# Kernel tuning notes

Measured on AMD Instinct MI355X. Metric: run time of the kernel, lower is better.

## Reference

```python
import jax, jax.numpy as jnp
import numpy as np

N_NODES = 100000
N_EDGES = 1600000
F = 64
UNITS = 64


def setup_inputs() -> dict:
    key = jax.random.key(0)
    k = jax.random.split(key, 8)
    x = jax.random.normal(k[0], (N_NODES, F), dtype=jnp.float32)
    edge_index = jax.random.randint(k[1], (2, N_EDGES), 0, N_NODES, dtype=jnp.int32)
    edge_weight = jnp.ones((N_EDGES,), dtype=jnp.float32)
    # glorot-uniform-ish params
    def glorot(kk, shape):
        lim = np.sqrt(6.0 / (shape[0] + shape[1]))
        return jax.random.uniform(kk, shape, dtype=jnp.float32, minval=-lim, maxval=lim)
    mlp_kernel = glorot(k[2], (F, UNITS))
    mlp_bias = jnp.zeros((UNITS,), dtype=jnp.float32)
    neighs_kernel = glorot(k[3], (UNITS, UNITS))
    self_kernel = glorot(k[4], (F, UNITS))
    bias = jnp.zeros((2 * UNITS,), dtype=jnp.float32)
    return {"x": x, "edge_index": edge_index, "edge_weight": edge_weight,
            "mlp_kernel": mlp_kernel, "mlp_bias": mlp_bias,
            "neighs_kernel": neighs_kernel, "self_kernel": self_kernel, "bias": bias}


def reference(x, edge_index, edge_weight, mlp_kernel, mlp_bias, neighs_kernel, self_kernel, bias):
    num_nodes = x.shape[0]
    row, col = edge_index[0], edge_index[1]
    # gcn_mapper: neighbor message scaled by edge weight (original forces weights to 1)
    neighbor_x = x[col] * edge_weight[:, None]            # [E, F]
    h = jax.nn.relu(neighbor_x @ mlp_kernel + mlp_bias)   # [E, U]
    # unsorted_segment_mean over destination row (empty segments -> 0, matching TF)
    seg_sum = jax.ops.segment_sum(h, row, num_segments=num_nodes)              # [N, U]
    cnt = jax.ops.segment_sum(jnp.ones_like(row, dtype=h.dtype), row, num_segments=num_nodes)
    reduced_h = seg_sum / jnp.maximum(cnt, 1.0)[:, None]
    from_neighs = reduced_h @ neighs_kernel               # [N, U]
    from_x = x @ self_kernel                              # [N, U]
    out = jnp.concatenate([from_neighs, from_x], axis=1) + bias
    out = jax.nn.relu(out)                                # [N, 2U]
    return out
```

## Files before the change

### kernel.cpp

```cpp
#include <hip/hip_runtime.h>

#define MAXSLICE 12544
#define MAXSUB   800
#define NBH 32
#define IDXCAP 512

static __device__ __forceinline__ float relu_f(float v) { return fmaxf(v, 0.f); }

static __device__ __forceinline__ unsigned short f2bf(float f) {
  unsigned u = __float_as_uint(f);
  u += 0x7fffu + ((u >> 16) & 1u);
  return (unsigned short)(u >> 16);
}
static __device__ __forceinline__ float bf2f(unsigned short h) {
  return __uint_as_float(((unsigned)h) << 16);
}

__global__ __launch_bounds__(256) void k_node_dual_gemm(
    const float* __restrict__ x, const float* __restrict__ mk,
    const float* __restrict__ sk, const float* __restrict__ bias,
    unsigned short* __restrict__ xwh, float* __restrict__ out, int n_nodes)
{
  __shared__ float s_mk[64][64];
  __shared__ float s_sk[64][64];
  __shared__ float s_xT[64][68];
  const int tid = threadIdx.x;
  for (int i = tid; i < 4096; i += 256) {
    s_mk[i >> 6][i & 63] = mk[i];
    s_sk[i >> 6][i & 63] = sk[i];
  }
  const int node0 = blockIdx.x * 64;
  for (int i = tid; i < 4096; i += 256) {
    int nl = i >> 6, f = i & 63;
    int n = node0 + nl;
    s_xT[f][nl] = (n < n_nodes) ? x[(size_t)n * 64 + f] : 0.f;
  }
  __syncthreads();
  const int g  = tid >> 4;
  const int ub = (tid & 15) * 4;
  float am[4][4] = {{0.f}};
  float as[4][4] = {{0.f}};
  for (int f = 0; f < 64; ++f) {
    float4 wm = *(const float4*)&s_mk[f][ub];
    float4 ws = *(const float4*)&s_sk[f][ub];
    float4 xv = *(const float4*)&s_xT[f][4 * g];
    const float xs[4] = {xv.x, xv.y, xv.z, xv.w};
#pragma unroll
    for (int j = 0; j < 4; ++j) {
      am[j][0] += xs[j] * wm.x; am[j][1] += xs[j] * wm.y;
      am[j][2] += xs[j] * wm.z; am[j][3] += xs[j] * wm.w;
      as[j][0] += xs[j] * ws.x; as[j][1] += xs[j] * ws.y;
      as[j][2] += xs[j] * ws.z; as[j][3] += xs[j] * ws.w;
    }
  }
  float4 bv = *(const float4*)&bias[64 + ub];
#pragma unroll
  for (int j = 0; j < 4; ++j) {
    int n = node0 + 4 * g + j;
    if (n >= n_nodes) break;
    ushort4 o1 = make_ushort4(f2bf(am[j][0]), f2bf(am[j][1]),
                              f2bf(am[j][2]), f2bf(am[j][3]));
    *(ushort4*)&xwh[(size_t)n * 64 + ub] = o1;
    *(float4*)&out[(size_t)n * 128 + 64 + ub] =
        make_float4(relu_f(as[j][0] + bv.x), relu_f(as[j][1] + bv.y),
                    relu_f(as[j][2] + bv.z), relu_f(as[j][3] + bv.w));
  }
}

__global__ __launch_bounds__(256) void k_count(
    const int* __restrict__ row, int* __restrict__ cnt, int n_edges)
{
  int e = blockIdx.x * 256 + threadIdx.x;
  if (e < n_edges) atomicAdd(&cnt[row[e]], 1);
}

__global__ __launch_bounds__(256) void k_build_sliced(
    const int* __restrict__ row, const int* __restrict__ col,
    const float* __restrict__ ew, int* __restrict__ off,
    int2* __restrict__ elist, int n_edges, int n_nodes)
{
  const int slice = blockIdx.x & 7;
  const int vb    = blockIdx.x >> 3;
  const int nvb   = gridDim.x >> 3;
  const int sliceN = (n_nodes + 7) >> 3;
  const int lo = slice * sliceN;
  const int hi = min(lo + sliceN, n_nodes);
  for (int e = vb * 256 + threadIdx.x; e < n_edges; e += nvb * 256) {
    int r = row[e];
    if (r >= lo && r < hi) {
      int pos = atomicAdd(&off[r], 1);
      elist[pos] = make_int2(col[e], __float_as_int(ew[e]));
    }
  }
}

__global__ __launch_bounds__(1024) void k_bsum(
    const int* __restrict__ cnt, int* __restrict__ bsum, int n)
{
  __shared__ int s[1024];
  int tid = threadIdx.x;
  int i = blockIdx.x * 1024 + tid;
  s[tid] = (i < n) ? cnt[i] : 0;
  __syncthreads();
  for (int d = 512; d > 0; d >>= 1) {
    if (tid < d) s[tid] += s[tid + d];
    __syncthreads();
  }
  if (tid == 0) bsum[blockIdx.x] = s[0];
}

__global__ __launch_bounds__(1024) void k_boffs(
    const int* __restrict__ cnt, const int* __restrict__ bsum,
    int* __restrict__ off, int n, int nb)
{
  __shared__ int s[1024];
  __shared__ int sp[128];
  int tid = threadIdx.x;
  if (tid < 128) {
    int acc = 0;
    for (int j = tid; j < blockIdx.x && j < nb; j += 128) acc += bsum[j];
    sp[tid] = acc;
  }
  int i = blockIdx.x * 1024 + tid;
  int v = (i < n) ? cnt[i] : 0;
  s[tid] = v;
  __syncthreads();
  for (int d = 64; d > 0; d >>= 1) {
    if (tid < d) sp[tid] += sp[tid + d];
    __syncthreads();
  }
  for (int d = 1; d < 1024; d <<= 1) {
    int t = (tid >= d) ? s[tid - d] : 0;
    __syncthreads();
    s[tid] += t;
    __syncthreads();
  }
  if (i < n) off[i] = s[tid] - v + sp[0];
}

__global__ __launch_bounds__(256) void k_bin(
    const int* __restrict__ row, const int* __restrict__ col,
    const float* __restrict__ ew,
    int* __restrict__ brow, int2* __restrict__ bpair,
    int* __restrict__ bcur, int n_edges, int sliceN, int cap)
{
  __shared__ int  s_wcnt[4][8];
  __shared__ int  s_tot[8];
  __shared__ int  s_toff[8];
  __shared__ int  s_gaddr[8];
  __shared__ int  s_rowst[1024];
  __shared__ int2 s_pairst[1024];
  const int tid  = threadIdx.x;
  const int wave = tid >> 6;
  const int lane = tid & 63;
  const unsigned usliceN = (unsigned)sliceN;
  const int stride = gridDim.x * 1024;
  for (int e0 = blockIdx.x * 1024; e0 < n_edges; e0 += stride) {
    const int e = e0 + 4 * tid;
    int   rr[4], cc[4];
    float ww[4];
    int   ss[4];
    if (e + 3 < n_edges) {
      int4 r4   = *(const int4*)&row[e];
      int4 c4   = *(const int4*)&col[e];
      float4 w4 = *(const float4*)&ew[e];
      rr[0] = r4.x; rr[1] = r4.y; rr[2] = r4.z; rr[3] = r4.w;
      cc[0] = c4.x; cc[1] = c4.y; cc[2] = c4.z; cc[3] = c4.w;
      ww[0] = w4.x; ww[1] = w4.y; ww[2] = w4.z; ww[3] = w4.w;
#pragma unroll
      for (int j = 0; j < 4; ++j) ss[j] = (int)((unsigned)rr[j] / usliceN);
    } else {
#pragma unroll
      for (int j = 0; j < 4; ++j) {
        int ej = e + j;
        bool v = ej < n_edges;
        rr[j] = v ? row[ej] : 0;
        cc[j] = v ? col[ej] : 0;
        ww[j] = v ? ew[ej]  : 0.f;
        ss[j] = v ? (int)((unsigned)rr[j] / usliceN) : -1;
      }
    }
#pragma unroll
    for (int b = 0; b < 8; ++b) {
      int c = 0;
#pragma unroll
      for (int j = 0; j < 4; ++j) c += __popcll(__ballot(ss[j] == b));
      if (lane == 0) s_wcnt[wave][b] = c;
    }
    __syncthreads();
    if (wave == 0 && lane < 8) {
      const int b = lane;
      int t0 = s_wcnt[0][b], t1 = s_wcnt[1][b], t2 = s_wcnt[2][b], t3 = s_wcnt[3][b];
      int tot = t0 + t1 + t2 + t3;
      s_tot[b] = tot;
      s_wcnt[0][b] = 0;
      s_wcnt[1][b] = t0;
      s_wcnt[2][b] = t0 + t1;
      s_wcnt[3][b] = t0 + t1 + t2;
      int gbase = tot ? atomicAdd(&bcur[b], tot) : 0;
      int pre = 0;
#pragma unroll
      for (int j2 = 0; j2 < 8; ++j2) pre += (j2 < b) ? s_tot[j2] : 0;
      s_toff[b]  = pre;
      s_gaddr[b] = b * cap + gbase - pre;
    }
    __syncthreads();
#pragma unroll
    for (int b = 0; b < 8; ++b) {
      const int sb = s_toff[b] + s_wcnt[wave][b];
      int off_local = 0;
#pragma unroll
      for (int j = 0; j < 4; ++j) {
        unsigned long long mm = __ballot(ss[j] == b);
        if (ss[j] == b) {
          int rank = __popcll(mm & ((1ull << lane) - 1ull));
          int slot = sb + off_local + rank;
          s_rowst[slot]  = rr[j];
          s_pairst[slot] = make_int2(cc[j], __float_as_int(ww[j]));
        }
        off_local += __popcll(mm);
      }
    }
    __syncthreads();
    const int total = s_toff[7] + s_tot[7];
    for (int i2 = tid; i2 < total; i2 += 256) {
      int b = 0;
#pragma unroll
      for (int j2 = 1; j2 < 8; ++j2) b += (i2 >= s_toff[j2]) ? 1 : 0;
      int a = s_gaddr[b] + i2;
      if (a < (b + 1) * cap) {
        brow[a]  = s_rowst[i2];
        bpair[a] = s_pairst[i2];
      }
    }
    __syncthreads();
  }
}

__global__ __launch_bounds__(256) void k_hist(
    const int* __restrict__ brow, const int* __restrict__ bcur,
    int* __restrict__ hist, int cap, int chunk, int sliceN)
{
  __shared__ int h[MAXSLICE];
  const int s   = blockIdx.x & 7;
  const int blk = blockIdx.x >> 3;
  const int tid = threadIdx.x;
  for (int i = tid; i < MAXSLICE; i += 256) h[i] = 0;
  __syncthreads();
  const int n_s  = min(bcur[s], cap);
  const int lo_e = blk * chunk;
  const int hi_e = min(lo_e + chunk, n_s);
  const int base = s * cap;
  const int lo   = s * sliceN;
  for (int i = lo_e + tid; i < hi_e; i += 256) {
    atomicAdd(&h[brow[base + i] - lo], 1);
  }
  __syncthreads();
  int* hrow = hist + (size_t)(s * NBH + blk) * MAXSLICE;
  for (int i = tid; i < MAXSLICE / 4; i += 256) {
    ((int4*)hrow)[i] = ((const int4*)h)[i];
  }
}

__global__ __launch_bounds__(256) void k_colscan(
    int* __restrict__ hist, int* __restrict__ cnt, int sliceN, int n_nodes)
{
  const int s  = blockIdx.x & 7;
  const int cb = blockIdx.x >> 3;
  const int b0 = cb * 1024 + threadIdx.x * 4;
  if (b0 >= sliceN) return;
  int4 acc = make_int4(0, 0, 0, 0);
  int* hs = hist + (size_t)s * NBH * MAXSLICE;
#pragma unroll 4
  for (int blk = 0; blk < NBH; ++blk) {
    int4* p = (int4*)(hs + (size_t)blk * MAXSLICE + b0);
    int4 v = *p;
    *p = acc;
    acc.x += v.x; acc.y += v.y; acc.z += v.z; acc.w += v.w;
  }
  const int node = s * sliceN + b0;
  if (b0 + 3 < sliceN && node + 3 < n_nodes) {
    *(int4*)&cnt[node] = acc;
  } else {
    int a[4] = {acc.x, acc.y, acc.z, acc.w};
    for (int j = 0; j < 4; ++j)
      if (b0 + j < sliceN && node + j < n_nodes) cnt[node + j] = a[j];
  }
}

__global__ __launch_bounds__(256) void k_place(
    const int* __restrict__ brow, const int2* __restrict__ bpair,
    const int* __restrict__ bcur, const int* __restrict__ hist,
    const int* __restrict__ off, int2* __restrict__ elist,
    int cap, int chunk, int sliceN, int n_nodes)
{
  __shared__ int cur[MAXSLICE];
  const int s   = blockIdx.x & 7;
  const int blk = blockIdx.x >> 3;
  const int tid = threadIdx.x;
  const int lo  = s * sliceN;
  const int hi  = min(lo + sliceN, n_nodes);
  const int nb  = hi - lo;
  const int* hrow = hist + (size_t)(s * NBH + blk) * MAXSLICE;
  for (int i = tid; i < nb; i += 256) cur[i] = off[lo + i] + hrow[i];
  __syncthreads();
  const int n_s  = min(bcur[s], cap);
  const int lo_e = blk * chunk;
  const int hi_e = min(lo_e + chunk, n_s);
  const int base = s * cap;
  for (int i = lo_e + tid; i < hi_e; i += 256) {
    int r = brow[base + i] - lo;
    int p = atomicAdd(&cur[r], 1);
    elist[p] = bpair[base + i];
  }
}

__global__ __launch_bounds__(256) void k_fused_csr(
    const int* __restrict__ cnt, const int* __restrict__ off,
    const int2* __restrict__ elist, const unsigned short* __restrict__ xwh,
    const float* __restrict__ mb, const float* __restrict__ nk,
    const float* __restrict__ bias, float* __restrict__ out, int n_nodes,
    int starts)
{
  __shared__ float s_nk[64][64];
  __shared__ float s_rh[16][68];
  const int tid = threadIdx.x;
  for (int i = tid; i < 1024; i += 256) {
    *(float4*)&s_nk[0][4 * i] = *(const float4*)&nk[4 * i];
  }
  const int node_l = tid >> 4;
  const int q = tid & 15;
  const int n = blockIdx.x * 16 + node_l;
  float4 acc = make_float4(0.f, 0.f, 0.f, 0.f);
  if (n < n_nodes) {
    const float4 mbq = *(const float4*)&mb[4 * q];
    const int c = cnt[n];
    int i = off[n] - (starts ? 0 : c);
    const int end = i + c;
    for (; i + 8 <= end; i += 8) {
      int2 e[8];
#pragma unroll
      for (int j = 0; j < 8; ++j) e[j] = elist[i + j];
      ushort4 u[8];
#pragma unroll
      for (int j = 0; j < 8; ++j)
        u[j] = *(const ushort4*)&xwh[(size_t)e[j].x * 64 + 4 * q];
#pragma unroll
      for (int j = 0; j < 8; ++j) {
        float w = __int_as_float(e[j].y);
        acc.x += relu_f(w * bf2f(u[j].x) + mbq.x);
        acc.y += relu_f(w * bf2f(u[j].y) + mbq.y);
        acc.z += relu_f(w * bf2f(u[j].z) + mbq.z);
        acc.w += relu_f(w * bf2f(u[j].w) + mbq.w);
      }
    }
    if (i + 4 <= end) {
      int2 e[4];
#pragma unroll
      for (int j = 0; j < 4; ++j) e[j] = elist[i + j];
      ushort4 u[4];
#pragma unroll
      for (int j = 0; j < 4; ++j)
        u[j] = *(const ushort4*)&xwh[(size_t)e[j].x * 64 + 4 * q];
#pragma unroll
      for (int j = 0; j < 4; ++j) {
        float w = __int_as_float(e[j].y);
        acc.x += relu_f(w * bf2f(u[j].x) + mbq.x);
        acc.y += relu_f(w * bf2f(u[j].y) + mbq.y);
        acc.z += relu_f(w * bf2f(u[j].z) + mbq.z);
        acc.w += relu_f(w * bf2f(u[j].w) + mbq.w);
      }
      i += 4;
    }
    for (; i < end; ++i) {
      int2 e0 = elist[i];
      ushort4 u0 = *(const ushort4*)&xwh[(size_t)e0.x * 64 + 4 * q];
      float w0 = __int_as_float(e0.y);
      acc.x += relu_f(w0 * bf2f(u0.x) + mbq.x);
      acc.y += relu_f(w0 * bf2f(u0.y) + mbq.y);
      acc.z += relu_f(w0 * bf2f(u0.z) + mbq.z);
      acc.w += relu_f(w0 * bf2f(u0.w) + mbq.w);
    }
    const float inv = 1.0f / fmaxf((float)c, 1.0f);
    acc.x *= inv; acc.y *= inv; acc.z *= inv; acc.w *= inv;
  }
  *(float4*)&s_rh[node_l][4 * q] = acc;
  __syncthreads();
  float4 o = make_float4(0.f, 0.f, 0.f, 0.f);
  for (int f = 0; f < 64; ++f) {
    float rv = s_rh[node_l][f];
    float4 wv = *(const float4*)&s_nk[f][4 * q];
    o.x += rv * wv.x; o.y += rv * wv.y; o.z += rv * wv.z; o.w += rv * wv.w;
  }
  if (n < n_nodes) {
    float4 bv = *(const float4*)&bias[4 * q];
    *(float4*)&out[(size_t)n * 128 + 4 * q] =
        make_float4(relu_f(o.x + bv.x), relu_f(o.y + bv.y),
                    relu_f(o.z + bv.z), relu_f(o.w + bv.w));
  }
}


__global__ __launch_bounds__(256) void k_hist16(
    const int* __restrict__ brow, const int* __restrict__ bcur,
    int* __restrict__ hist, int cap, int chunk, int sliceN)
{
  __shared__ int h[MAXSUB];
  const int s   = blockIdx.x & 7;
  const int blk = blockIdx.x >> 3;
  const int tid = threadIdx.x;
  const int nsub = (sliceN + 15) >> 4;
  for (int i = tid; i < nsub; i += 256) h[i] = 0;
  __syncthreads();
  const int n_s  = min(bcur[s], cap);
  const int lo_e = blk * chunk;
  const int hi_e = min(lo_e + chunk, n_s);
  const int base = s * cap;
  const int lo   = s * sliceN;
  for (int i = lo_e + tid; i < hi_e; i += 256) {
    atomicAdd(&h[(brow[base + i] - lo) >> 4], 1);
  }
  __syncthreads();
  int* hrow = hist + (size_t)(s * NBH + blk) * MAXSUB;
  for (int i = tid; i < nsub; i += 256) hrow[i] = h[i];
}

__global__ __launch_bounds__(1024) void k_colscan16(
    int* __restrict__ hist, const int* __restrict__ bcur,
    int* __restrict__ off_sub, int cap, int sliceN)
{
  __shared__ int s_t[1024];
  const int s = blockIdx.x;
  const int tid = threadIdx.x;
  const int nsub = (sliceN + 15) >> 4;
  int acc = 0;
  if (tid < nsub) {
    int* hs = hist + (size_t)s * NBH * MAXSUB;
    for (int blk = 0; blk < NBH; ++blk) {
      int* p = hs + (size_t)blk * MAXSUB + tid;
      int v = *p;
      *p = acc;
      acc += v;
    }
  }
  s_t[tid] = (tid < nsub) ? acc : 0;
  __syncthreads();
  for (int d = 1; d < 1024; d <<= 1) {
    int t = (tid >= d) ? s_t[tid - d] : 0;
    __syncthreads();
    s_t[tid] += t;
    __syncthreads();
  }
  int base = 0;
  for (int b = 0; b < s; ++b) base += min(bcur[b], cap);
  int excl = (tid == 0) ? 0 : s_t[tid - 1];
  if (tid < nsub) off_sub[s * nsub + tid] = base + excl;
  if (s == 7 && tid == 1023) off_sub[8 * nsub] = base + s_t[1023];
}

__global__ __launch_bounds__(256) void k_place16(
    const int* __restrict__ brow, const int2* __restrict__ bpair,
    const int* __restrict__ bcur, const int* __restrict__ hist,
    const int* __restrict__ off_sub, int2* __restrict__ elist,
    int cap, int chunk, int sliceN)
{
  __shared__ int cur[MAXSUB];
  const int s   = blockIdx.x & 7;
  const int blk = blockIdx.x >> 3;
  const int tid = threadIdx.x;
  const int nsub = (sliceN + 15) >> 4;
  const int* hrow = hist + (size_t)(s * NBH + blk) * MAXSUB;
  for (int i = tid; i < nsub; i += 256) cur[i] = off_sub[s * nsub + i] + hrow[i];
  __syncthreads();
  const int n_s  = min(bcur[s], cap);
  const int lo_e = blk * chunk;
  const int hi_e = min(lo_e + chunk, n_s);
  const int base = s * cap;
  const int lo   = s * sliceN;
  for (int i = lo_e + tid; i < hi_e; i += 256) {
    int rloc = brow[base + i] - lo;
    int p = atomicAdd(&cur[rloc >> 4], 1);
    int2 pr = bpair[base + i];
    elist[p] = make_int2(pr.x | ((rloc & 15) << 27), pr.y);
  }
}

__global__ __launch_bounds__(256) void k_fused_sub(
    const int* __restrict__ osub, const int2* __restrict__ elist,
    const unsigned short* __restrict__ xwh, const float* __restrict__ mb,
    const float* __restrict__ nk, const float* __restrict__ bias,
    float* __restrict__ out, int n_nodes, int sliceN)
{
  __shared__ float s_nk[64][64];
  __shared__ float s_rh[16][68];
  __shared__ int s_h[16];
  __shared__ int s_pre[17];
  __shared__ int s_cur[16];
  __shared__ unsigned short s_idx[IDXCAP];
  const int tid = threadIdx.x;
  for (int i = tid; i < 1024; i += 256) {
    *(float4*)&s_nk[0][4 * i] = *(const float4*)&nk[4 * i];
  }
  const int s   = blockIdx.x & 7;
  const int sub = blockIdx.x >> 3;
  const int nsub = (sliceN + 15) >> 4;
  const int e0 = osub[s * nsub + sub];
  const int e1 = osub[s * nsub + sub + 1];
  const int g = tid >> 4;
  const int q = tid & 15;
  const float4 mbq = *(const float4*)&mb[4 * q];
  float4 acc = make_float4(0.f, 0.f, 0.f, 0.f);
  int cnt_g = 0;
  for (int c0 = e0; c0 < e1; c0 += IDXCAP) {
    const int m = min(IDXCAP, e1 - c0);
    if (tid < 16) s_h[tid] = 0;
    __syncthreads();
    for (int i = tid; i < m; i += 256) {
      atomicAdd(&s_h[((unsigned)elist[c0 + i].x) >> 27], 1);
    }
    __syncthreads();
    if (tid == 0) {
      int a = 0;
#pragma unroll
      for (int b = 0; b < 16; ++b) { s_pre[b] = a; s_cur[b] = a; a += s_h[b]; }
      s_pre[16] = a;
    }
    __syncthreads();
    for (int i = tid; i < m; i += 256) {
      int rl = ((unsigned)elist[c0 + i].x) >> 27;
      int p = atomicAdd(&s_cur[rl], 1);
      s_idx[p] = (unsigned short)i;
    }
    __syncthreads();
    const int st = s_pre[g];
    const int cN = s_h[g];
    cnt_g += cN;
    int k = 0;
    for (; k + 8 <= cN; k += 8) {
      int2 e[8];
#pragma unroll
      for (int j = 0; j < 8; ++j) e[j] = elist[c0 + s_idx[st + k + j]];
      ushort4 u[8];
#pragma unroll
      for (int j = 0; j < 8; ++j)
        u[j] = *(const ushort4*)&xwh[(size_t)(e[j].x & 0x07FFFFFF) * 64 + 4 * q];
#pragma unroll
      for (int j = 0; j < 8; ++j) {
        float w = __int_as_float(e[j].y);
        acc.x += relu_f(w * bf2f(u[j].x) + mbq.x);
        acc.y += relu_f(w * bf2f(u[j].y) + mbq.y);
        acc.z += relu_f(w * bf2f(u[j].z) + mbq.z);
        acc.w += relu_f(w * bf2f(u[j].w) + mbq.w);
      }
    }
    if (k + 4 <= cN) {
      int2 e[4];
#pragma unroll
      for (int j = 0; j < 4; ++j) e[j] = elist[c0 + s_idx[st + k + j]];
      ushort4 u[4];
#pragma unroll
      for (int j = 0; j < 4; ++j)
        u[j] = *(const ushort4*)&xwh[(size_t)(e[j].x & 0x07FFFFFF) * 64 + 4 * q];
#pragma unroll
      for (int j = 0; j < 4; ++j) {
        float w = __int_as_float(e[j].y);
        acc.x += relu_f(w * bf2f(u[j].x) + mbq.x);
        acc.y += relu_f(w * bf2f(u[j].y) + mbq.y);
        acc.z += relu_f(w * bf2f(u[j].z) + mbq.z);
        acc.w += relu_f(w * bf2f(u[j].w) + mbq.w);
      }
      k += 4;
    }
    for (; k < cN; ++k) {
      int2 ev = elist[c0 + s_idx[st + k]];
      ushort4 u0 = *(const ushort4*)&xwh[(size_t)(ev.x & 0x07FFFFFF) * 64 + 4 * q];
      float w = __int_as_float(ev.y);
      acc.x += relu_f(w * bf2f(u0.x) + mbq.x);
      acc.y += relu_f(w * bf2f(u0.y) + mbq.y);
      acc.z += relu_f(w * bf2f(u0.z) + mbq.z);
      acc.w += relu_f(w * bf2f(u0.w) + mbq.w);
    }
    __syncthreads();
  }
  const float inv = 1.0f / fmaxf((float)cnt_g, 1.0f);
  acc.x *= inv; acc.y *= inv; acc.z *= inv; acc.w *= inv;
  *(float4*)&s_rh[g][4 * q] = acc;
  __syncthreads();
  float4 o = make_float4(0.f, 0.f, 0.f, 0.f);
  for (int f = 0; f < 64; ++f) {
    float rv = s_rh[g][f];
    float4 wv = *(const float4*)&s_nk[f][4 * q];
    o.x += rv * wv.x; o.y += rv * wv.y; o.z += rv * wv.z; o.w += rv * wv.w;
  }
  const int loc = sub * 16 + g;
  const int n = s * sliceN + loc;
  if (loc < sliceN && n < n_nodes) {
    float4 bv = *(const float4*)&bias[4 * q];
    *(float4*)&out[(size_t)n * 128 + 4 * q] =
        make_float4(relu_f(o.x + bv.x), relu_f(o.y + bv.y),
                    relu_f(o.z + bv.z), relu_f(o.w + bv.w));
  }
}

extern "C" void kernel_launch(void* const* d_in, const int* in_sizes, int n_in,
                              void* d_out, int out_size, void* d_ws, size_t ws_size,
                              hipStream_t stream) {
  const float* x    = (const float*)d_in[0];
  const int*   ei   = (const int*)d_in[1];
  const float* ew   = (const float*)d_in[2];
  const float* mk   = (const float*)d_in[3];
  const float* mb   = (const float*)d_in[4];
  const float* nk   = (const float*)d_in[5];
  const float* sk   = (const float*)d_in[6];
  const float* bias = (const float*)d_in[7];
  float* out = (float*)d_out;

  const int n_nodes = in_sizes[0] / 64;
  const int n_edges = in_sizes[2];
  const int* row = ei;
  const int* col = ei + n_edges;

  unsigned short* xwh = (unsigned short*)d_ws;
  int*  cnt  = (int*)(xwh + (size_t)n_nodes * 64);
  int*  bcur = cnt + n_nodes;
  int*  off  = bcur + 8;
  int*  bsum = off + n_nodes;
  int*  osub = bsum + 128;
  size_t ebytes = ((size_t)((char*)(osub + 8 * MAXSUB + 8) - (char*)d_ws) + 7) & ~(size_t)7;
  int2* elist = (int2*)((char*)d_ws + ebytes);
  const int cap = (n_edges >> 3) + 8192;
  int*  brow  = (int*)(elist + n_edges);
  size_t pboff = (((size_t)((char*)(brow + (size_t)8 * cap) - (char*)d_ws)) + 7) & ~(size_t)7;
  int2* bpair = (int2*)((char*)d_ws + pboff);
  size_t need_b = (size_t)((char*)(bpair + (size_t)8 * cap) - (char*)d_ws);
  size_t hoff = (need_b + 15) & ~(size_t)15;
  int*  hist  = (int*)((char*)d_ws + hoff);
  size_t need_a = hoff + (size_t)8 * NBH * MAXSLICE * sizeof(int);

  const int nb_scan = (n_nodes + 1023) / 1024;
  const int sliceN = (n_nodes + 7) >> 3;
  const int nsub = (sliceN + 15) >> 4;
  const int nbn = (n_nodes + 63) / 64;
  const int nbf = (n_nodes + 15) / 16;
  const int chunk = (cap + NBH - 1) / NBH;

  const bool fitsA = (ws_size >= need_a) && (sliceN <= MAXSLICE);
  const bool subOK = fitsA && (nsub <= MAXSUB) && (n_nodes >= 16) &&
                     (n_nodes < (1 << 27)) && ((size_t)8 * cap >= (size_t)n_edges);

  if (subOK) {
    hipMemsetAsync(bcur, 0, 8 * sizeof(int), stream);
    k_node_dual_gemm<<<nbn, 256, 0, stream>>>(x, mk, sk, bias, xwh, out, n_nodes);
    int nbb = (n_edges + 1023) / 1024;
    if (nbb > 2048) nbb = 2048;
    k_bin<<<nbb, 256, 0, stream>>>(row, col, ew, brow, bpair, bcur,
                                   n_edges, sliceN, cap);
    k_hist16<<<8 * NBH, 256, 0, stream>>>(brow, bcur, hist, cap, chunk, sliceN);
    k_colscan16<<<8, 1024, 0, stream>>>(hist, bcur, osub, cap, sliceN);
    k_place16<<<8 * NBH, 256, 0, stream>>>(brow, bpair, bcur, hist, osub,
                                           elist, cap, chunk, sliceN);
    k_fused_sub<<<8 * nsub, 256, 0, stream>>>(osub, elist, xwh, mb, nk, bias,
                                              out, n_nodes, sliceN);
  } else if (fitsA) {
    hipMemsetAsync(bcur, 0, 8 * sizeof(int), stream);
    k_node_dual_gemm<<<nbn, 256, 0, stream>>>(x, mk, sk, bias, xwh, out, n_nodes);
    int nbb = (n_edges + 1023) / 1024;
    if (nbb > 2048) nbb = 2048;
    k_bin<<<nbb, 256, 0, stream>>>(row, col, ew, brow, bpair, bcur,
                                   n_edges, sliceN, cap);
    k_hist<<<8 * NBH, 256, 0, stream>>>(brow, bcur, hist, cap, chunk, sliceN);
    const int ncb = (sliceN + 1023) / 1024;
    k_colscan<<<8 * ncb, 256, 0, stream>>>(hist, cnt, sliceN, n_nodes);
    k_bsum<<<nb_scan, 1024, 0, stream>>>(cnt, bsum, n_nodes);
    k_boffs<<<nb_scan, 1024, 0, stream>>>(cnt, bsum, off, n_nodes, nb_scan);
    k_place<<<8 * NBH, 256, 0, stream>>>(brow, bpair, bcur, hist, off,
                                         elist, cap, chunk, sliceN, n_nodes);
    k_fused_csr<<<nbf, 256, 0, stream>>>(cnt, off, elist, xwh, mb, nk,
                                         bias, out, n_nodes, 1);
  } else {
    hipMemsetAsync(cnt, 0, (size_t)n_nodes * sizeof(int), stream);
    k_node_dual_gemm<<<nbn, 256, 0, stream>>>(x, mk, sk, bias, xwh, out, n_nodes);
    const int nbe = (n_edges + 255) / 256;
    k_count<<<nbe, 256, 0, stream>>>(row, cnt, n_edges);
    k_bsum<<<nb_scan, 1024, 0, stream>>>(cnt, bsum, n_nodes);
    k_boffs<<<nb_scan, 1024, 0, stream>>>(cnt, bsum, off, n_nodes, nb_scan);
    k_build_sliced<<<1024, 256, 0, stream>>>(row, col, ew, off, elist,
                                             n_edges, n_nodes);
    k_fused_csr<<<nbf, 256, 0, stream>>>(cnt, off, elist, xwh, mb, nk,
                                         bias, out, n_nodes, 0);
  }
}
```

Measured before the change: 253.2 us.

## Fuse edge binning, histogram, scan and placement into one cooperative kernel

Replaces the memset plus four launches (bin, hist16, colscan16, place16) with a single cooperative kernel that uses grid-wide syncs between phases, keeping the same algorithm. The goal is to cut per-kernel launch and drain overhead along the CSR-build chain. In exchange, the grid is capped at occupancy-limited resident blocks (at most 1024), so the 8-job colscan phase leaves most blocks idle and grid.sync has its own cost. If the cooperative launch fails, the code falls back to the old multi-kernel path.

```diff
diff --git a/kernel.cpp b/kernel.cpp
--- a/kernel.cpp
+++ b/kernel.cpp
@@ -1,9 +1,12 @@
 #include <hip/hip_runtime.h>
+#include <hip/hip_cooperative_groups.h>
 
 #define MAXSLICE 12544
 #define MAXSUB   800
 #define NBH 32
 #define IDXCAP 512
+
+namespace cg = cooperative_groups;
 
 static __device__ __forceinline__ float relu_f(float v) { return fmaxf(v, 0.f); }
 
@@ -237,6 +240,200 @@
   }
 }
 
+__global__ __launch_bounds__(256) void k_build_coop(
+    const int* __restrict__ row, const int* __restrict__ col,
+    const float* __restrict__ ew,
+    int* __restrict__ brow, int2* __restrict__ bpair, int* __restrict__ bcur,
+    int* __restrict__ hist, int* __restrict__ osub, int2* __restrict__ elist,
+    int n_edges, int sliceN, int cap)
+{
+  __shared__ union {
+    struct { int wcnt[4][8]; int tot[8]; int toff[8]; int gaddr[8];
+             int rowst[1024]; int2 pairst[1024]; } bin;
+    struct { int h[MAXSUB]; } hs;
+    struct { int tot[MAXSUB]; int part[256]; } sc;
+    struct { int cur[MAXSUB]; } pl;
+  } u;
+  cg::grid_group grid = cg::this_grid();
+  const int tid = threadIdx.x;
+  const int bid = blockIdx.x;
+  const int nb  = gridDim.x;
+  const int nsub = (sliceN + 15) >> 4;
+  const int chunk = (cap + NBH - 1) / NBH;
+
+  if (bid == 0 && tid < 8) bcur[tid] = 0;
+  grid.sync();
+
+  {
+    const int wave = tid >> 6;
+    const int lane = tid & 63;
+    const unsigned usliceN = (unsigned)sliceN;
+    const int stride = nb * 1024;
+    for (int e0 = bid * 1024; e0 < n_edges; e0 += stride) {
+      const int e = e0 + 4 * tid;
+      int   rr[4], cc[4];
+      float ww[4];
+      int   ss[4];
+      if (e + 3 < n_edges) {
+        int4 r4   = *(const int4*)&row[e];
+        int4 c4   = *(const int4*)&col[e];
+        float4 w4 = *(const float4*)&ew[e];
+        rr[0] = r4.x; rr[1] = r4.y; rr[2] = r4.z; rr[3] = r4.w;
+        cc[0] = c4.x; cc[1] = c4.y; cc[2] = c4.z; cc[3] = c4.w;
+        ww[0] = w4.x; ww[1] = w4.y; ww[2] = w4.z; ww[3] = w4.w;
+#pragma unroll
+        for (int j = 0; j < 4; ++j) ss[j] = (int)((unsigned)rr[j] / usliceN);
+      } else {
+#pragma unroll
+        for (int j = 0; j < 4; ++j) {
+          int ej = e + j;
+          bool v = ej < n_edges;
+          rr[j] = v ? row[ej] : 0;
+          cc[j] = v ? col[ej] : 0;
+          ww[j] = v ? ew[ej]  : 0.f;
+          ss[j] = v ? (int)((unsigned)rr[j] / usliceN) : -1;
+        }
+      }
+#pragma unroll
+      for (int b = 0; b < 8; ++b) {
+        int c = 0;
+#pragma unroll
+        for (int j = 0; j < 4; ++j) c += __popcll(__ballot(ss[j] == b));
+        if (lane == 0) u.bin.wcnt[wave][b] = c;
+      }
+      __syncthreads();
+      if (wave == 0 && lane < 8) {
+        const int b = lane;
+        int t0 = u.bin.wcnt[0][b], t1 = u.bin.wcnt[1][b];
+        int t2 = u.bin.wcnt[2][b], t3 = u.bin.wcnt[3][b];
+        int tot = t0 + t1 + t2 + t3;
+        u.bin.tot[b] = tot;
+        u.bin.wcnt[0][b] = 0;
+        u.bin.wcnt[1][b] = t0;
+        u.bin.wcnt[2][b] = t0 + t1;
+        u.bin.wcnt[3][b] = t0 + t1 + t2;
+        int gbase = tot ? atomicAdd(&bcur[b], tot) : 0;
+        int pre = 0;
+#pragma unroll
+        for (int j2 = 0; j2 < 8; ++j2) pre += (j2 < b) ? u.bin.tot[j2] : 0;
+        u.bin.toff[b]  = pre;
+        u.bin.gaddr[b] = b * cap + gbase - pre;
+      }
+      __syncthreads();
+#pragma unroll
+      for (int b = 0; b < 8; ++b) {
+        const int sb = u.bin.toff[b] + u.bin.wcnt[wave][b];
+        int off_local = 0;
+#pragma unroll
+        for (int j = 0; j < 4; ++j) {
+          unsigned long long mm = __ballot(ss[j] == b);
+          if (ss[j] == b) {
+            int rank = __popcll(mm & ((1ull << lane) - 1ull));
+            int slot = sb + off_local + rank;
+            u.bin.rowst[slot]  = rr[j];
+            u.bin.pairst[slot] = make_int2(cc[j], __float_as_int(ww[j]));
+          }
+          off_local += __popcll(mm);
+        }
+      }
+      __syncthreads();
+      const int total = u.bin.toff[7] + u.bin.tot[7];
+      for (int i2 = tid; i2 < total; i2 += 256) {
+        int b = 0;
+#pragma unroll
+        for (int j2 = 1; j2 < 8; ++j2) b += (i2 >= u.bin.toff[j2]) ? 1 : 0;
+        int a = u.bin.gaddr[b] + i2;
+        if (a < (b + 1) * cap) {
+          brow[a]  = u.bin.rowst[i2];
+          bpair[a] = u.bin.pairst[i2];
+        }
+      }
+      __syncthreads();
+    }
+  }
+  grid.sync();
+
+  for (int job = bid; job < 8 * NBH; job += nb) {
+    const int s = job & 7, blk = job >> 3;
+    for (int i = tid; i < nsub; i += 256) u.hs.h[i] = 0;
+    __syncthreads();
+    const int n_s  = min(bcur[s], cap);
+    const int lo_e = blk * chunk;
+    const int hi_e = min(lo_e + chunk, n_s);
+    const int base = s * cap;
+    const int lo   = s * sliceN;
+    for (int i = lo_e + tid; i < hi_e; i += 256) {
+      atomicAdd(&u.hs.h[(brow[base + i] - lo) >> 4], 1);
+    }
+    __syncthreads();
+    int* hrow = hist + (size_t)(s * NBH + blk) * MAXSUB;
+    for (int i = tid; i < nsub; i += 256) hrow[i] = u.hs.h[i];
+    __syncthreads();
+  }
+  grid.sync();
+
+  for (int job = bid; job < 8; job += nb) {
+    const int s = job;
+    int* hsl = hist + (size_t)s * NBH * MAXSUB;
+    for (int i = tid; i < nsub; i += 256) {
+      int acc = 0;
+      for (int blk = 0; blk < NBH; ++blk) {
+        int* p = hsl + (size_t)blk * MAXSUB + i;
+        int v = *p; *p = acc; acc += v;
+      }
+      u.sc.tot[i] = acc;
+    }
+    __syncthreads();
+    const int G = (nsub + 255) >> 8;
+    const int base_i = tid * G;
+    int vals[4]; int locsum = 0;
+#pragma unroll
+    for (int j = 0; j < 4; ++j) {
+      int i = base_i + j;
+      int v = (j < G && i < nsub) ? u.sc.tot[i] : 0;
+      vals[j] = locsum; locsum += v;
+    }
+    u.sc.part[tid] = locsum;
+    __syncthreads();
+    for (int d = 1; d < 256; d <<= 1) {
+      int t = (tid >= d) ? u.sc.part[tid - d] : 0;
+      __syncthreads();
+      u.sc.part[tid] += t;
+      __syncthreads();
+    }
+    int segpre = (tid == 0) ? 0 : u.sc.part[tid - 1];
+    int sbase = 0;
+    for (int b = 0; b < s; ++b) sbase += min(bcur[b], cap);
+#pragma unroll
+    for (int j = 0; j < 4; ++j) {
+      int i = base_i + j;
+      if (j < G && i < nsub) osub[s * nsub + i] = sbase + segpre + vals[j];
+    }
+    if (s == 7 && tid == 255) osub[8 * nsub] = sbase + u.sc.part[255];
+    __syncthreads();
+  }
+  grid.sync();
+
+  for (int job = bid; job < 8 * NBH; job += nb) {
+    const int s = job & 7, blk = job >> 3;
+    const int* hrow = hist + (size_t)(s * NBH + blk) * MAXSUB;
+    for (int i = tid; i < nsub; i += 256) u.pl.cur[i] = osub[s * nsub + i] + hrow[i];
+    __syncthreads();
+    const int n_s  = min(bcur[s], cap);
+    const int lo_e = blk * chunk;
+    const int hi_e = min(lo_e + chunk, n_s);
+    const int base = s * cap;
+    const int lo   = s * sliceN;
+    for (int i = lo_e + tid; i < hi_e; i += 256) {
+      int rloc = brow[base + i] - lo;
+      int p = atomicAdd(&u.pl.cur[rloc >> 4], 1);
+      int2 pr = bpair[base + i];
+      elist[p] = make_int2(pr.x | ((rloc & 15) << 27), pr.y);
+    }
+    __syncthreads();
+  }
+}
+
 __global__ __launch_bounds__(256) void k_hist(
     const int* __restrict__ brow, const int* __restrict__ bcur,
     int* __restrict__ hist, int cap, int chunk, int sliceN)
@@ -399,7 +596,6 @@
                     relu_f(o.z + bv.z), relu_f(o.w + bv.w));
   }
 }
-
 
 __global__ __launch_bounds__(256) void k_hist16(
     const int* __restrict__ brow, const int* __restrict__ bcur,
@@ -648,7 +844,52 @@
   const bool subOK = fitsA && (nsub <= MAXSUB) && (n_nodes >= 16) &&
                      (n_nodes < (1 << 27)) && ((size_t)8 * cap >= (size_t)n_edges);
 
-  if (subOK) {
+  static int coop_blocks = -1;
+  if (coop_blocks < 0) {
+    int dev = 0, attr = 0;
+    hipGetDevice(&dev);
+    hipDeviceGetAttribute(&attr, hipDeviceAttributeCooperativeLaunch, dev);
+    if (attr) {
+      int nbmp = 0, mp = 0;
+      if (hipOccupancyMaxActiveBlocksPerMultiprocessor(&nbmp, k_build_coop, 256, 0)
+          != hipSuccess) nbmp = 0;
+      hipDeviceGetAttribute(&mp, hipDeviceAttributeMultiprocessorCount, dev);
+      coop_blocks = (nbmp > 0 && mp > 0) ? nbmp * mp : 0;
+    } else {
+      coop_blocks = 0;
+    }
+  }
+
+  bool done = false;
+  if (subOK && coop_blocks >= 8) {
+    k_node_dual_gemm<<<nbn, 256, 0, stream>>>(x, mk, sk, bias, xwh, out, n_nodes);
+    int g = coop_blocks < 1024 ? coop_blocks : 1024;
+    void* kargs[] = {(void*)&row, (void*)&col, (void*)&ew, (void*)&brow,
+                     (void*)&bpair, (void*)&bcur, (void*)&hist, (void*)&osub,
+                     (void*)&elist, (void*)&n_edges, (void*)&sliceN, (void*)&cap};
+    hipError_t e = hipLaunchCooperativeKernel((void*)k_build_coop, dim3(g),
+                                              dim3(256), kargs, 0, stream);
+    if (e == hipSuccess) {
+      k_fused_sub<<<8 * nsub, 256, 0, stream>>>(osub, elist, xwh, mb, nk, bias,
+                                                out, n_nodes, sliceN);
+      done = true;
+    } else {
+      hipMemsetAsync(bcur, 0, 8 * sizeof(int), stream);
+      int nbb = (n_edges + 1023) / 1024;
+      if (nbb > 2048) nbb = 2048;
+      k_bin<<<nbb, 256, 0, stream>>>(row, col, ew, brow, bpair, bcur,
+                                     n_edges, sliceN, cap);
+      k_hist16<<<8 * NBH, 256, 0, stream>>>(brow, bcur, hist, cap, chunk, sliceN);
+      k_colscan16<<<8, 1024, 0, stream>>>(hist, bcur, osub, cap, sliceN);
+      k_place16<<<8 * NBH, 256, 0, stream>>>(brow, bpair, bcur, hist, osub,
+                                             elist, cap, chunk, sliceN);
+      k_fused_sub<<<8 * nsub, 256, 0, stream>>>(osub, elist, xwh, mb, nk, bias,
+                                                out, n_nodes, sliceN);
+      done = true;
+    }
+  }
+
+  if (!done && subOK) {
     hipMemsetAsync(bcur, 0, 8 * sizeof(int), stream);
     k_node_dual_gemm<<<nbn, 256, 0, stream>>>(x, mk, sk, bias, xwh, out, n_nodes);
     int nbb = (n_edges + 1023) / 1024;
@@ -661,7 +902,10 @@
                                            elist, cap, chunk, sliceN);
     k_fused_sub<<<8 * nsub, 256, 0, stream>>>(osub, elist, xwh, mb, nk, bias,
                                               out, n_nodes, sliceN);
-  } else if (fitsA) {
+    done = true;
+  }
+
+  if (!done && fitsA) {
     hipMemsetAsync(bcur, 0, 8 * sizeof(int), stream);
     k_node_dual_gemm<<<nbn, 256, 0, stream>>>(x, mk, sk, bias, xwh, out, n_nodes);
     int nbb = (n_edges + 1023) / 1024;
@@ -677,7 +921,10 @@
                                          elist, cap, chunk, sliceN, n_nodes);
     k_fused_csr<<<nbf, 256, 0, stream>>>(cnt, off, elist, xwh, mb, nk,
                                          bias, out, n_nodes, 1);
-  } else {
+    done = true;
+  }
+
+  if (!done) {
     hipMemsetAsync(cnt, 0, (size_t)n_nodes * sizeof(int), stream);
     k_node_dual_gemm<<<nbn, 256, 0, stream>>>(x, mk, sk, bias, xwh, out, n_nodes);
     const int nbe = (n_edges + 255) / 256;
```

Measured after the change: 544.9 us. 115% more time.
